# Performance work log

Measured on AMD Instinct MI355X. Metric: run time of the kernel, lower is better.

The kernel has to match this reference:

```python
import jax, jax.numpy as jnp
import numpy as np

N = 64           # protein_length
B = 32           # batch
L = 2 * N - 1    # lattice side = 127


def setup_inputs() -> dict:
    key = jax.random.key(0)
    k1, k2, k3 = jax.random.split(key, 3)
    acids = jax.random.normal(k1, (B, N), dtype=jnp.float32)
    # raw indices in [0, N-1]; after +(N-1) shift they land in [N-1, 2N-2] < L
    idx = jax.random.randint(k2, (B, N, 3), 0, N, dtype=jnp.int32)
    mask = jax.random.bernoulli(k3, 0.7, (B, N))
    return {"acids": acids, "idx": idx, "mask": mask}


def reference(acids, idx, mask):
    # acids: (B,N) f32, idx: (B,N,3) int, mask: (B,N) bool
    shifted = idx + (N - 1)                       # center lattice at N-1
    vals = jnp.where(mask, acids, jnp.float32(0)) # masked-off acids scatter 0 (no-op under add)
    b = jnp.broadcast_to(jnp.arange(B)[:, None], (B, N))
    lattice = jnp.zeros((B, L, L, L), dtype=jnp.float32)
    # single fused batched scatter (replaces per-sample tf.map_fn + sparse_to_dense)
    lattice = lattice.at[b, shifted[..., 0], shifted[..., 1], shifted[..., 2]].add(vals)
    return lattice
```

## Files before the change

kernel.cpp:

```cpp
#include <hip/hip_runtime.h>


constexpr int PN = 64;
constexpr int PB = 32;
constexpr int PL = 2 * PN - 1;

__global__ void lattice_scatter_kernel(const float* __restrict__ acids,
                                       const int*   __restrict__ idx,
                                       const int*   __restrict__ mask,
                                       float*       __restrict__ out) {
    int t = blockIdx.x * blockDim.x + threadIdx.x;
    if (t >= PB * PN) return;
    if (mask[t] == 0) return;
    float v = acids[t];
    int b = t >> 6;
    int i0 = idx[3 * t + 0] + (PN - 1);
    int i1 = idx[3 * t + 1] + (PN - 1);
    int i2 = idx[3 * t + 2] + (PN - 1);
    size_t off = ((((size_t)b * PL + i0) * PL) + i1) * PL + i2;
    atomicAdd(out + off, v);
}

extern "C" void kernel_launch(void* const* d_in, const int* in_sizes, int n_in,
                              void* d_out, int out_size, void* d_ws, size_t ws_size,
                              hipStream_t stream) {
    const float* acids = (const float*)d_in[0];
    const int*   idx   = (const int*)  d_in[1];
    const int*   mask  = (const int*)  d_in[2];
    float* out = (float*)d_out;

    hipMemsetAsync(out, 0, (size_t)out_size, stream);

    constexpr int total = PB * PN;
    lattice_scatter_kernel<<<(total + 255) / 256, 256, 0, stream>>>(acids, idx, mask, out);
}
```

Measured before the change: 224.6 us.

## Fuse lattice zero-fill and scatter into one vectorized write kernel

Replaces the memset plus atomic scatter with a single kernel in which each block owns a contiguous chunk of the output. The block first gathers the masked points that land in its chunk into shared memory, then writes its chunk once with float4 stores, adding any matching point values in registers. This removes the separate memset pass and the global atomics. The cost is that every block scans all 2048 points, and blocks that hold points run an inner loop over those points for each vector they store.

Measured after the change: 268.2 us. +19.4%, slower.

```diff
diff --git a/kernel.cpp b/kernel.cpp
--- a/kernel.cpp
+++ b/kernel.cpp
@@ -4,21 +4,71 @@
 constexpr int PN = 64;
 constexpr int PB = 32;
 constexpr int PL = 2 * PN - 1;
+constexpr long long TOTAL_F = (long long)PB * PL * PL * PL;
+constexpr long long TOTAL_V4 = TOTAL_F / 4;
+constexpr int NPTS = PB * PN;
 
-__global__ void lattice_scatter_kernel(const float* __restrict__ acids,
-                                       const int*   __restrict__ idx,
-                                       const int*   __restrict__ mask,
-                                       float*       __restrict__ out) {
-    int t = blockIdx.x * blockDim.x + threadIdx.x;
-    if (t >= PB * PN) return;
-    if (mask[t] == 0) return;
-    float v = acids[t];
-    int b = t >> 6;
-    int i0 = idx[3 * t + 0] + (PN - 1);
-    int i1 = idx[3 * t + 1] + (PN - 1);
-    int i2 = idx[3 * t + 2] + (PN - 1);
-    size_t off = ((((size_t)b * PL + i0) * PL) + i1) * PL + i2;
-    atomicAdd(out + off, v);
+constexpr int FB = 256;
+constexpr int FGRID = 2048;
+constexpr int CH = (int)((TOTAL_V4 + FGRID - 1) / FGRID);
+
+typedef float v4f __attribute__((ext_vector_type(4)));
+
+__global__ __launch_bounds__(FB) void lattice_fused_kernel(
+        const float* __restrict__ acids,
+        const int*   __restrict__ idx,
+        const int*   __restrict__ mask,
+        v4f*         __restrict__ out) {
+    __shared__ int   s_cnt;
+    __shared__ int   s_off[NPTS];
+    __shared__ float s_val[NPTS];
+
+    const int tid = threadIdx.x;
+    const long long lo = (long long)blockIdx.x * CH;
+    long long hi = lo + CH;
+    if (hi > TOTAL_V4) hi = TOTAL_V4;
+    if (tid == 0) s_cnt = 0;
+    __syncthreads();
+
+    const long long elo = lo * 4, ehi = hi * 4;
+    for (int p = tid; p < NPTS; p += FB) {
+        if (mask[p] != 0) {
+            long long b  = p >> 6;
+            long long i0 = idx[3 * p + 0] + (PN - 1);
+            long long i1 = idx[3 * p + 1] + (PN - 1);
+            long long i2 = idx[3 * p + 2] + (PN - 1);
+            long long off = ((b * PL + i0) * PL + i1) * PL + i2;
+            if (off >= elo && off < ehi) {
+                int slot = atomicAdd(&s_cnt, 1);
+                s_off[slot] = (int)off;
+                s_val[slot] = acids[p];
+            }
+        }
+    }
+    __syncthreads();
+    const int n = s_cnt;
+
+    if (n == 0) {
+        const v4f z = {0.f, 0.f, 0.f, 0.f};
+        for (long long t = lo + tid; t < hi; t += FB)
+            out[t] = z;
+    } else {
+        for (long long t = lo + tid; t < hi; t += FB) {
+            v4f z = {0.f, 0.f, 0.f, 0.f};
+            const int e0 = (int)(t << 2);
+            for (int k = 0; k < n; ++k) {
+                int d = s_off[k] - e0;
+                if ((unsigned)d < 4u) {
+                    float v = s_val[k];
+                    if      (d == 0) z.x += v;
+                    else if (d == 1) z.y += v;
+                    else if (d == 2) z.z += v;
+                    else             z.w += v;
+                }
+            }
+            out[t] = z;
+        }
+    }
 }
 
 extern "C" void kernel_launch(void* const* d_in, const int* in_sizes, int n_in,
@@ -29,8 +79,5 @@
     const int*   mask  = (const int*)  d_in[2];
     float* out = (float*)d_out;
 
-    hipMemsetAsync(out, 0, (size_t)out_size, stream);
-
-    constexpr int total = PB * PN;
-    lattice_scatter_kernel<<<(total + 255) / 256, 256, 0, stream>>>(acids, idx, mask, out);
+    lattice_fused_kernel<<<FGRID, FB, 0, stream>>>(acids, idx, mask, (v4f*)out);
 }
```
